# Performance work log

Hardware: AMD Instinct MI355X
Metric: run time of the kernel (lower is better)

## Reference

```python
import jax, jax.numpy as jnp
import numpy as np

TEMP = 0.05
EPS = 1e-6


def _l2norm(x):
    return x / jnp.linalg.norm(x, axis=1, keepdims=True)


def setup_inputs() -> dict:
    key = jax.random.key(0)
    k1, k2, k3, k4 = jax.random.split(key, 4)
    B, D = 4096, 768
    return {
        "feat": jax.random.normal(k1, (B, D), dtype=jnp.float32),
        "feat_gen": jax.random.normal(k2, (B, D), dtype=jnp.float32),
        "feat_aug": jax.random.normal(k3, (B, D), dtype=jnp.float32),
        "targets": jax.random.randint(k4, (B,), 0, 100, dtype=jnp.int64),
    }


def reference(feat, feat_gen, feat_aug, targets):
    B = feat.shape[0]
    on = _l2norm(feat)
    gn = _l2norm(feat_gen)
    an = _l2norm(feat_aug)
    # [B, B] exp-similarity matrices
    exp_ori = jnp.exp(on @ on.T / TEMP)
    exp_gen = jnp.exp(on @ gn.T / TEMP)
    exp_aug = jnp.exp(on @ an.T / TEMP)

    same = (targets[:, None] == targets[None, :])  # [B, B] bool, includes diagonal
    same_f = same.astype(exp_ori.dtype)

    # ---- co loss: anchors vs ori+aug columns ----
    oa = exp_ori + exp_aug
    diff_sum_oa = oa.sum(axis=1) - (oa * same_f).sum(axis=1)        # [B]
    denom_co = diff_sum_oa + exp_gen.sum(axis=1) + EPS              # [B]
    term_o = -jnp.log(exp_ori / (exp_ori + denom_co[:, None]) + EPS)
    term_a = -jnp.log(exp_aug / (exp_aug + denom_co[:, None]) + EPS)
    co_loss = ((term_o + term_a) * same_f).sum() / B

    # ---- ad loss: anchors vs gen columns ----
    diff_sum_g = exp_gen.sum(axis=1) - (exp_gen * same_f).sum(axis=1)
    denom_ad = diff_sum_g + exp_aug.sum(axis=1) + exp_ori.sum(axis=1) + EPS
    term_g = -jnp.log(exp_gen / (exp_gen + denom_ad[:, None]) + EPS)
    ad_loss = (term_g * same_f).sum() / B

    return (ad_loss, co_loss)
```

## Files before the change

### kernel.cpp

```cpp
#include <hip/hip_runtime.h>
#include <hip/hip_bf16.h>
#include <math.h>

#define Bn 4096
#define Dd 768
#define SC2 28.85390081777927f
#define EPSF 1e-6f
#define DG 4.8516519541e8f

#define O_S      0
#define O_SMOA   12288
#define O_SMG    16384
#define ZERO_F   20480
#define O_P      20480
#define O_RM     20608
#define LIST_OFF   262144
#define LCAP       (1u << 19)
#define NB_OFF     33554432

typedef __attribute__((ext_vector_type(8))) short sh8;
typedef __attribute__((ext_vector_type(4))) float f32x4;

#define AS1 __attribute__((address_space(1)))
#define AS3 __attribute__((address_space(3)))

static __device__ __forceinline__ void gl_lds16(const void* g, void* l) {
    __builtin_amdgcn_global_load_lds((const AS1 void*)g, (AS3 void*)l, 16, 0, 0);
}

static __device__ __forceinline__ unsigned short f2b(float f) {
    unsigned int u = __float_as_uint(f);
    unsigned int r = (u + 0x7fffu + ((u >> 16) & 1u)) >> 16;
    return (unsigned short)r;
}

__global__ void norm_kernel(const float* f0, const float* f1, const float* f2, unsigned short* nb) {
    int r = blockIdx.x, m = blockIdx.y, tid = threadIdx.x;
    const float* src = (m == 0 ? f0 : (m == 1 ? f1 : f2)) + (size_t)r * Dd;
    float x0 = src[tid], x1 = src[tid + 256], x2 = src[tid + 512];
    float v = x0 * x0 + x1 * x1 + x2 * x2;
    #pragma unroll
    for (int off = 1; off < 64; off <<= 1) v += __shfl_xor(v, off);
    __shared__ float wr[4];
    if ((tid & 63) == 0) wr[tid >> 6] = v;
    __syncthreads();
    float inv = rsqrtf(wr[0] + wr[1] + wr[2] + wr[3]);
    unsigned short* dst = nb + ((size_t)m * Bn + r) * Dd;
    dst[tid] = f2b(x0 * inv);
    dst[tid + 256] = f2b(x1 * inv);
    dst[tid + 512] = f2b(x2 * inv);
}

__launch_bounds__(1024)
__global__ void sort_kernel(const int* tg, unsigned int* I, float* out) {
    float* F = (float*)I;
    __shared__ unsigned int h[128], pb[128], cur[128];
    int tid = threadIdx.x;
    for (int e = tid; e < ZERO_F; e += 1024) F[e] = 0.f;
    if (tid == 0) { out[0] = 0.f; out[1] = 0.f; }
    if (tid < 128) { h[tid] = 0; cur[tid] = 0; }
    __syncthreads();
    for (int e = tid; e < Bn; e += 1024) atomicAdd(&h[tg[e]], 1u);
    __syncthreads();
    if (tid < 128) pb[tid] = h[tid] * h[tid];
    __syncthreads();
    for (int s = 1; s < 128; s <<= 1) {
        unsigned int b = 0;
        if (tid < 128 && tid >= s) b = pb[tid - s];
        __syncthreads();
        if (tid < 128) pb[tid] += b;
        __syncthreads();
    }
    if (tid == 127) I[O_P] = pb[127];
    uint2* RM = (uint2*)(I + O_RM);
    for (int e = tid; e < Bn; e += 1024) {
        int c = tg[e];
        unsigned int r = atomicAdd(&cur[c], 1u);
        unsigned int n = h[c];
        RM[e] = make_uint2((unsigned)c | (r << 8), (pb[c] - n * n) + r * n);
    }
}

__launch_bounds__(256, 4)
__global__ void gemm_rowsum(const unsigned short* nb, char* ws) {
    float* F = (float*)ws;
    const unsigned int* I = (const unsigned int*)ws;
    const uint2* RM = (const uint2*)(I + O_RM);
    int z = blockIdx.z;
    const unsigned short* Ag = nb;
    const unsigned short* Bg = nb + (size_t)z * Bn * Dd;
    int m0 = blockIdx.y * 128, n0 = blockIdx.x * 128;
    int tid = threadIdx.x, lane = tid & 63, wave = tid >> 6;
    int wm = (wave >> 1) * 64, wn = (wave & 1) * 64;
    int lid = lane & 15, q = lane >> 4;
    __shared__ __align__(16) unsigned short Asm[128 * 32];
    __shared__ __align__(16) unsigned short Bsm[128 * 32];
    int c0 = tid, c1 = tid + 256;
    int row0 = c0 >> 2, sg0 = (c0 & 3) ^ ((row0 >> 1) & 3);
    int row1 = c1 >> 2, sg1 = (c1 & 3) ^ ((row1 >> 1) & 3);
    const unsigned short* gA0 = Ag + (size_t)(m0 + row0) * Dd + sg0 * 8;
    const unsigned short* gA1 = Ag + (size_t)(m0 + row1) * Dd + sg1 * 8;
    const unsigned short* gB0 = Bg + (size_t)(n0 + row0) * Dd + sg0 * 8;
    const unsigned short* gB1 = Bg + (size_t)(n0 + row1) * Dd + sg1 * 8;
    unsigned short* lA0 = &Asm[c0 * 8];
    unsigned short* lA1 = &Asm[c1 * 8];
    unsigned short* lB0 = &Bsm[c0 * 8];
    unsigned short* lB1 = &Bsm[c1 * 8];
    f32x4 acc[4][4] = {};
    for (int kt = 0; kt < Dd / 32; ++kt) {
        __syncthreads();
        gl_lds16(gA0 + kt * 32, lA0);
        gl_lds16(gA1 + kt * 32, lA1);
        gl_lds16(gB0 + kt * 32, lB0);
        gl_lds16(gB1 + kt * 32, lB1);
        __syncthreads();
        sh8 af[4], bf[4];
        #pragma unroll
        for (int i = 0; i < 4; ++i) {
            int r = wm + i * 16 + lid;
            af[i] = *(const sh8*)&Asm[r * 32 + ((q ^ ((r >> 1) & 3)) * 8)];
        }
        #pragma unroll
        for (int j = 0; j < 4; ++j) {
            int r = wn + j * 16 + lid;
            bf[j] = *(const sh8*)&Bsm[r * 32 + ((q ^ ((r >> 1) & 3)) * 8)];
        }
        #pragma unroll
        for (int i = 0; i < 4; ++i)
            #pragma unroll
            for (int j = 0; j < 4; ++j)
                acc[i][j] = __builtin_amdgcn_mfma_f32_16x16x32_bf16(af[i], bf[j], acc[i][j], 0, 0, 0);
    }
    uint2 rmc[4];
    #pragma unroll
    for (int j = 0; j < 4; ++j) rmc[j] = RM[n0 + wn + j * 16 + lid];
    int smoff = (z == 1) ? O_SMG : O_SMOA;
    unsigned int* Lw = (unsigned int*)(ws + LIST_OFF);
    #pragma unroll
    for (int i = 0; i < 4; ++i)
        #pragma unroll
        for (int reg = 0; reg < 4; ++reg) {
            int grow = m0 + wm + i * 16 + q * 4 + reg;
            uint2 rm = RM[grow];
            unsigned int trow = rm.x & 255u, rsb = rm.y;
            float rs = 0.f, ms = 0.f;
            #pragma unroll
            for (int j = 0; j < 4; ++j) {
                int gcol = n0 + wn + j * 16 + lid;
                float x = acc[i][j][reg] * SC2;
                float e = exp2f(x);
                if (z == 0 && gcol == grow) e = 0.f;
                rs += e;
                if ((rmc[j].x & 255u) == trow) {
                    ms += e;
                    unsigned int slot = rsb + (rmc[j].x >> 8);
                    if (slot < LCAP) {
                        if (z == 0) {
                            Lw[slot * 4 + 0] = (unsigned)grow;
                            Lw[slot * 4 + 1] = __float_as_uint(x);
                        } else {
                            Lw[slot * 4 + 1 + z] = __float_as_uint(x);
                        }
                    }
                }
            }
            #pragma unroll
            for (int off = 1; off < 16; off <<= 1) {
                rs += __shfl_xor(rs, off);
                ms += __shfl_xor(ms, off);
            }
            if (lid == 0) {
                atomicAdd(&F[O_S + z * Bn + grow], rs);
                atomicAdd(&F[smoff + grow], ms);
            }
        }
}

__launch_bounds__(256)
__global__ void loss_kernel(char* ws, float* out) {
    float* F = (float*)ws;
    const unsigned int* I = (const unsigned int*)ws;
    const uint4* L = (const uint4*)(ws + LIST_OFF);
    unsigned int n = I[O_P]; if (n > LCAP) n = LCAP;
    float a0 = 0.f, a1 = 0.f;
    unsigned int stride = gridDim.x * 256;
    for (unsigned int idx = blockIdx.x * 256 + threadIdx.x; idx < n; idx += stride) {
        uint4 en = L[idx];
        int i = (int)en.x;
        float son = F[O_S + i], sgen = F[O_S + Bn + i], saug = F[O_S + 2 * Bn + i];
        float dco = (son + saug - F[O_SMOA + i]) + sgen + EPSF;
        float dad = (sgen - F[O_SMG + i]) + saug + son + DG + EPSF;
        float eo = exp2f(__uint_as_float(en.y));
        float eg = exp2f(__uint_as_float(en.z));
        float ea = exp2f(__uint_as_float(en.w));
        a0 += -__logf(eg / (eg + dad) + EPSF);
        a1 += -__logf(eo / (eo + dco) + EPSF) - __logf(ea / (ea + dco) + EPSF);
    }
    #pragma unroll
    for (int off = 1; off < 64; off <<= 1) { a0 += __shfl_xor(a0, off); a1 += __shfl_xor(a1, off); }
    __shared__ float r0[4], r1[4];
    int tid = threadIdx.x;
    if ((tid & 63) == 0) { r0[tid >> 6] = a0; r1[tid >> 6] = a1; }
    __syncthreads();
    if (tid == 0) {
        atomicAdd(&out[0], (r0[0] + r0[1] + r0[2] + r0[3]) * (1.0f / Bn));
        atomicAdd(&out[1], (r1[0] + r1[1] + r1[2] + r1[3]) * (1.0f / Bn));
    }
}

extern "C" void kernel_launch(void* const* d_in, const int* in_sizes, int n_in,
                              void* d_out, int out_size, void* d_ws, size_t ws_size,
                              hipStream_t stream) {
    const float* f0 = (const float*)d_in[0];
    const float* f1 = (const float*)d_in[1];
    const float* f2 = (const float*)d_in[2];
    const int* tg = (const int*)d_in[3];
    char* ws = (char*)d_ws;
    unsigned int* I = (unsigned int*)d_ws;
    unsigned short* nb = (unsigned short*)(ws + NB_OFF);
    float* out = (float*)d_out;

    norm_kernel<<<dim3(Bn, 3), 256, 0, stream>>>(f0, f1, f2, nb);
    sort_kernel<<<1, 1024, 0, stream>>>(tg, I, out);
    gemm_rowsum<<<dim3(32, 32, 3), 256, 0, stream>>>(nb, ws);
    loss_kernel<<<256, 256, 0, stream>>>(ws, out);
}
```

Measured before the change: 221.2 us.

## Enlarge GEMM tile to 256x256 with 4-stage async LDS pipeline

The fused similarity GEMM moves from 128x128 tiles with 256 threads to 256x256 tiles with 512 threads. Each wave now computes 128x64. K-slices are prefetched three steps ahead into four LDS buffers, using explicit vmcnt waits and one barrier per step instead of two. MFMA blocks are wrapped in setprio. This aims to raise operand reuse and hide global-to-LDS latency, at the cost of 128 KB of LDS per block, more accumulator registers, and fewer blocks (768) to spread across CUs.

After: 256.1 us. 1.16x slower.

```diff
diff --git a/kernel.cpp b/kernel.cpp
--- a/kernel.cpp
+++ b/kernel.cpp
@@ -81,7 +81,7 @@
     }
 }
 
-__launch_bounds__(256, 4)
+__launch_bounds__(512, 2)
 __global__ void gemm_rowsum(const unsigned short* nb, char* ws) {
     float* F = (float*)ws;
     const unsigned int* I = (const unsigned int*)ws;
@@ -89,55 +89,74 @@
     int z = blockIdx.z;
     const unsigned short* Ag = nb;
     const unsigned short* Bg = nb + (size_t)z * Bn * Dd;
-    int m0 = blockIdx.y * 128, n0 = blockIdx.x * 128;
+    int m0 = blockIdx.y * 256, n0 = blockIdx.x * 256;
     int tid = threadIdx.x, lane = tid & 63, wave = tid >> 6;
-    int wm = (wave >> 1) * 64, wn = (wave & 1) * 64;
+    int wm = (wave >> 2) * 128, wn = (wave & 3) * 64;
     int lid = lane & 15, q = lane >> 4;
-    __shared__ __align__(16) unsigned short Asm[128 * 32];
-    __shared__ __align__(16) unsigned short Bsm[128 * 32];
-    int c0 = tid, c1 = tid + 256;
-    int row0 = c0 >> 2, sg0 = (c0 & 3) ^ ((row0 >> 1) & 3);
-    int row1 = c1 >> 2, sg1 = (c1 & 3) ^ ((row1 >> 1) & 3);
-    const unsigned short* gA0 = Ag + (size_t)(m0 + row0) * Dd + sg0 * 8;
-    const unsigned short* gA1 = Ag + (size_t)(m0 + row1) * Dd + sg1 * 8;
-    const unsigned short* gB0 = Bg + (size_t)(n0 + row0) * Dd + sg0 * 8;
-    const unsigned short* gB1 = Bg + (size_t)(n0 + row1) * Dd + sg1 * 8;
-    unsigned short* lA0 = &Asm[c0 * 8];
-    unsigned short* lA1 = &Asm[c1 * 8];
-    unsigned short* lB0 = &Bsm[c0 * 8];
-    unsigned short* lB1 = &Bsm[c1 * 8];
-    f32x4 acc[4][4] = {};
-    for (int kt = 0; kt < Dd / 32; ++kt) {
-        __syncthreads();
-        gl_lds16(gA0 + kt * 32, lA0);
-        gl_lds16(gA1 + kt * 32, lA1);
-        gl_lds16(gB0 + kt * 32, lB0);
-        gl_lds16(gB1 + kt * 32, lB1);
-        __syncthreads();
-        sh8 af[4], bf[4];
-        #pragma unroll
-        for (int i = 0; i < 4; ++i) {
+    __shared__ __align__(16) unsigned short Asm[4][256 * 32];
+    __shared__ __align__(16) unsigned short Bsm[4][256 * 32];
+
+    int r0 = tid >> 2, c0 = tid & 3;
+    int sg = (c0 ^ ((r0 >> 1) & 3)) * 8;
+    const unsigned short* pA0 = Ag + (size_t)(m0 + r0) * Dd + sg;
+    const unsigned short* pA1 = pA0 + (size_t)128 * Dd;
+    const unsigned short* pB0 = Bg + (size_t)(n0 + r0) * Dd + sg;
+    const unsigned short* pB1 = pB0 + (size_t)128 * Dd;
+
+    f32x4 acc[8][4] = {};
+
+    #pragma unroll
+    for (int p = 0; p < 3; ++p) {
+        gl_lds16(pA0 + p * 32, &Asm[p][tid * 8]);
+        gl_lds16(pA1 + p * 32, &Asm[p][(512 + tid) * 8]);
+        gl_lds16(pB0 + p * 32, &Bsm[p][tid * 8]);
+        gl_lds16(pB1 + p * 32, &Bsm[p][(512 + tid) * 8]);
+    }
+    pA0 += 96; pA1 += 96; pB0 += 96; pB1 += 96;
+
+    for (int kt = 0; kt < 24; ++kt) {
+        int buf = kt & 3;
+        if (kt < 22)       asm volatile("s_waitcnt vmcnt(8)" ::: "memory");
+        else if (kt == 22) asm volatile("s_waitcnt vmcnt(4)" ::: "memory");
+        else               asm volatile("s_waitcnt vmcnt(0)" ::: "memory");
+        __builtin_amdgcn_sched_barrier(0);
+        __builtin_amdgcn_s_barrier();
+        __builtin_amdgcn_sched_barrier(0);
+        if (kt < 21) {
+            int nbuf = (kt + 3) & 3;
+            gl_lds16(pA0, &Asm[nbuf][tid * 8]);
+            gl_lds16(pA1, &Asm[nbuf][(512 + tid) * 8]);
+            gl_lds16(pB0, &Bsm[nbuf][tid * 8]);
+            gl_lds16(pB1, &Bsm[nbuf][(512 + tid) * 8]);
+            pA0 += 32; pA1 += 32; pB0 += 32; pB1 += 32;
+        }
+        sh8 af[8], bf[4];
+        #pragma unroll
+        for (int i = 0; i < 8; ++i) {
             int r = wm + i * 16 + lid;
-            af[i] = *(const sh8*)&Asm[r * 32 + ((q ^ ((r >> 1) & 3)) * 8)];
+            af[i] = *(const sh8*)&Asm[buf][r * 32 + ((q ^ ((r >> 1) & 3)) * 8)];
         }
         #pragma unroll
         for (int j = 0; j < 4; ++j) {
             int r = wn + j * 16 + lid;
-            bf[j] = *(const sh8*)&Bsm[r * 32 + ((q ^ ((r >> 1) & 3)) * 8)];
-        }
-        #pragma unroll
-        for (int i = 0; i < 4; ++i)
+            bf[j] = *(const sh8*)&Bsm[buf][r * 32 + ((q ^ ((r >> 1) & 3)) * 8)];
+        }
+        __builtin_amdgcn_s_setprio(1);
+        #pragma unroll
+        for (int i = 0; i < 8; ++i)
             #pragma unroll
             for (int j = 0; j < 4; ++j)
                 acc[i][j] = __builtin_amdgcn_mfma_f32_16x16x32_bf16(af[i], bf[j], acc[i][j], 0, 0, 0);
-    }
+        __builtin_amdgcn_s_setprio(0);
+    }
+
     uint2 rmc[4];
     #pragma unroll
     for (int j = 0; j < 4; ++j) rmc[j] = RM[n0 + wn + j * 16 + lid];
     int smoff = (z == 1) ? O_SMG : O_SMOA;
     unsigned int* Lw = (unsigned int*)(ws + LIST_OFF);
     #pragma unroll
-    for (int i = 0; i < 4; ++i)
+    for (int i = 0; i < 8; ++i)
         #pragma unroll
         for (int reg = 0; reg < 4; ++reg) {
             int grow = m0 + wm + i * 16 + q * 4 + reg;
@@ -222,6 +241,6 @@
 
     norm_kernel<<<dim3(Bn, 3), 256, 0, stream>>>(f0, f1, f2, nb);
     sort_kernel<<<1, 1024, 0, stream>>>(tg, I, out);
-    gemm_rowsum<<<dim3(32, 32, 3), 256, 0, stream>>>(nb, ws);
+    gemm_rowsum<<<dim3(16, 16, 3), 512, 0, stream>>>(nb, ws);
     loss_kernel<<<256, 256, 0, stream>>>(ws, out);
 }
```

## Fuse three similarity GEMMs into one block sharing the anchor tile

Applied to the files above, without the earlier changes.

Each block now computes the ori, gen and aug similarity tiles together and loads the anchor A tile once for all three, where before the z dimension launched separate blocks. The epilogue computes all three row sums and same-class sums in one pass and writes each list entry as a single uint4 store instead of scattered partial writes. A swizzled 1D block index is added to improve L2 locality. In exchange the block holds three sets of accumulators (48 f32x4 each), so register pressure rises, launch bounds drop to 2 blocks per SIMD, and there are fewer blocks to spread over the CUs.

New measurement: 205.4 us. 1.08x faster.

```diff
diff --git a/kernel.cpp b/kernel.cpp
--- a/kernel.cpp
+++ b/kernel.cpp
@@ -81,61 +81,91 @@
     }
 }
 
-__launch_bounds__(256, 4)
+__launch_bounds__(256, 2)
 __global__ void gemm_rowsum(const unsigned short* nb, char* ws) {
     float* F = (float*)ws;
     const unsigned int* I = (const unsigned int*)ws;
     const uint2* RM = (const uint2*)(I + O_RM);
-    int z = blockIdx.z;
-    const unsigned short* Ag = nb;
-    const unsigned short* Bg = nb + (size_t)z * Bn * Dd;
-    int m0 = blockIdx.y * 128, n0 = blockIdx.x * 128;
+    int bid = blockIdx.x;
+    int sw = (bid & 7) * 128 + (bid >> 3);
+    int m0 = (sw >> 5) * 128, n0 = (sw & 31) * 128;
     int tid = threadIdx.x, lane = tid & 63, wave = tid >> 6;
     int wm = (wave >> 1) * 64, wn = (wave & 1) * 64;
     int lid = lane & 15, q = lane >> 4;
     __shared__ __align__(16) unsigned short Asm[128 * 32];
-    __shared__ __align__(16) unsigned short Bsm[128 * 32];
-    int c0 = tid, c1 = tid + 256;
-    int row0 = c0 >> 2, sg0 = (c0 & 3) ^ ((row0 >> 1) & 3);
-    int row1 = c1 >> 2, sg1 = (c1 & 3) ^ ((row1 >> 1) & 3);
-    const unsigned short* gA0 = Ag + (size_t)(m0 + row0) * Dd + sg0 * 8;
-    const unsigned short* gA1 = Ag + (size_t)(m0 + row1) * Dd + sg1 * 8;
-    const unsigned short* gB0 = Bg + (size_t)(n0 + row0) * Dd + sg0 * 8;
-    const unsigned short* gB1 = Bg + (size_t)(n0 + row1) * Dd + sg1 * 8;
-    unsigned short* lA0 = &Asm[c0 * 8];
-    unsigned short* lA1 = &Asm[c1 * 8];
-    unsigned short* lB0 = &Bsm[c0 * 8];
-    unsigned short* lB1 = &Bsm[c1 * 8];
-    f32x4 acc[4][4] = {};
-    for (int kt = 0; kt < Dd / 32; ++kt) {
-        __syncthreads();
-        gl_lds16(gA0 + kt * 32, lA0);
-        gl_lds16(gA1 + kt * 32, lA1);
-        gl_lds16(gB0 + kt * 32, lB0);
-        gl_lds16(gB1 + kt * 32, lB1);
-        __syncthreads();
-        sh8 af[4], bf[4];
-        #pragma unroll
-        for (int i = 0; i < 4; ++i) {
-            int r = wm + i * 16 + lid;
-            af[i] = *(const sh8*)&Asm[r * 32 + ((q ^ ((r >> 1) & 3)) * 8)];
-        }
-        #pragma unroll
-        for (int j = 0; j < 4; ++j) {
-            int r = wn + j * 16 + lid;
-            bf[j] = *(const sh8*)&Bsm[r * 32 + ((q ^ ((r >> 1) & 3)) * 8)];
-        }
+    __shared__ __align__(16) unsigned short Bsm[3][128 * 32];
+
+    int row0 = tid >> 2, ch = tid & 3;
+    int cs = (ch ^ ((row0 >> 1) & 3)) * 8;
+    const unsigned short* gA  = nb + (size_t)(m0 + row0) * Dd + cs;
+    const unsigned short* gB0 = nb + (size_t)(n0 + row0) * Dd + cs;
+    const unsigned short* gB1 = gB0 + (size_t)Bn * Dd;
+    const unsigned short* gB2 = gB1 + (size_t)Bn * Dd;
+    unsigned short* lA0 = &Asm[tid * 8];
+    unsigned short* lA1 = &Asm[(tid + 256) * 8];
+
+    int cswz = (q ^ ((lid >> 1) & 3)) * 8;
+
+    f32x4 a0[4][4] = {}, a1[4][4] = {}, a2[4][4] = {};
+
+    for (int kt = 0; kt < 24; ++kt) {
+        const unsigned short* pa  = gA  + kt * 32;
+        const unsigned short* pb0 = gB0 + kt * 32;
+        const unsigned short* pb1 = gB1 + kt * 32;
+        const unsigned short* pb2 = gB2 + kt * 32;
+        __syncthreads();
+        gl_lds16(pa, lA0);
+        gl_lds16(pa + (size_t)64 * Dd, lA1);
+        gl_lds16(pb0, &Bsm[0][tid * 8]);
+        gl_lds16(pb0 + (size_t)64 * Dd, &Bsm[0][(tid + 256) * 8]);
+        gl_lds16(pb1, &Bsm[1][tid * 8]);
+        gl_lds16(pb1 + (size_t)64 * Dd, &Bsm[1][(tid + 256) * 8]);
+        gl_lds16(pb2, &Bsm[2][tid * 8]);
+        gl_lds16(pb2 + (size_t)64 * Dd, &Bsm[2][(tid + 256) * 8]);
+        __syncthreads();
+        sh8 af[4];
         #pragma unroll
         for (int i = 0; i < 4; ++i)
+            af[i] = *(const sh8*)&Asm[(wm + i * 16 + lid) * 32 + cswz];
+        {
+            sh8 bf[4];
             #pragma unroll
             for (int j = 0; j < 4; ++j)
-                acc[i][j] = __builtin_amdgcn_mfma_f32_16x16x32_bf16(af[i], bf[j], acc[i][j], 0, 0, 0);
-    }
+                bf[j] = *(const sh8*)&Bsm[0][(wn + j * 16 + lid) * 32 + cswz];
+            #pragma unroll
+            for (int i = 0; i < 4; ++i)
+                #pragma unroll
+                for (int j = 0; j < 4; ++j)
+                    a0[i][j] = __builtin_amdgcn_mfma_f32_16x16x32_bf16(af[i], bf[j], a0[i][j], 0, 0, 0);
+        }
+        {
+            sh8 bf[4];
+            #pragma unroll
+            for (int j = 0; j < 4; ++j)
+                bf[j] = *(const sh8*)&Bsm[1][(wn + j * 16 + lid) * 32 + cswz];
+            #pragma unroll
+            for (int i = 0; i < 4; ++i)
+                #pragma unroll
+                for (int j = 0; j < 4; ++j)
+                    a1[i][j] = __builtin_amdgcn_mfma_f32_16x16x32_bf16(af[i], bf[j], a1[i][j], 0, 0, 0);
+        }
+        {
+            sh8 bf[4];
+            #pragma unroll
+            for (int j = 0; j < 4; ++j)
+                bf[j] = *(const sh8*)&Bsm[2][(wn + j * 16 + lid) * 32 + cswz];
+            #pragma unroll
+            for (int i = 0; i < 4; ++i)
+                #pragma unroll
+                for (int j = 0; j < 4; ++j)
+                    a2[i][j] = __builtin_amdgcn_mfma_f32_16x16x32_bf16(af[i], bf[j], a2[i][j], 0, 0, 0);
+        }
+    }
+
     uint2 rmc[4];
     #pragma unroll
     for (int j = 0; j < 4; ++j) rmc[j] = RM[n0 + wn + j * 16 + lid];
-    int smoff = (z == 1) ? O_SMG : O_SMOA;
-    unsigned int* Lw = (unsigned int*)(ws + LIST_OFF);
+    uint4* Lq = (uint4*)(ws + LIST_OFF);
     #pragma unroll
     for (int i = 0; i < 4; ++i)
         #pragma unroll
@@ -143,35 +173,41 @@
             int grow = m0 + wm + i * 16 + q * 4 + reg;
             uint2 rm = RM[grow];
             unsigned int trow = rm.x & 255u, rsb = rm.y;
-            float rs = 0.f, ms = 0.f;
+            float rs0 = 0.f, rs1 = 0.f, rs2 = 0.f, msOA = 0.f, msG = 0.f;
             #pragma unroll
             for (int j = 0; j < 4; ++j) {
                 int gcol = n0 + wn + j * 16 + lid;
-                float x = acc[i][j][reg] * SC2;
-                float e = exp2f(x);
-                if (z == 0 && gcol == grow) e = 0.f;
-                rs += e;
+                float x0 = a0[i][j][reg] * SC2;
+                float x1 = a1[i][j][reg] * SC2;
+                float x2 = a2[i][j][reg] * SC2;
+                float e0 = exp2f(x0);
+                float e1 = exp2f(x1);
+                float e2 = exp2f(x2);
+                if (gcol == grow) e0 = 0.f;
+                rs0 += e0; rs1 += e1; rs2 += e2;
                 if ((rmc[j].x & 255u) == trow) {
-                    ms += e;
+                    msOA += e0 + e2;
+                    msG  += e1;
                     unsigned int slot = rsb + (rmc[j].x >> 8);
-                    if (slot < LCAP) {
-                        if (z == 0) {
-                            Lw[slot * 4 + 0] = (unsigned)grow;
-                            Lw[slot * 4 + 1] = __float_as_uint(x);
-                        } else {
-                            Lw[slot * 4 + 1 + z] = __float_as_uint(x);
-                        }
-                    }
+                    if (slot < LCAP)
+                        Lq[slot] = make_uint4((unsigned)grow, __float_as_uint(x0),
+                                              __float_as_uint(x1), __float_as_uint(x2));
                 }
             }
             #pragma unroll
             for (int off = 1; off < 16; off <<= 1) {
-                rs += __shfl_xor(rs, off);
-                ms += __shfl_xor(ms, off);
+                rs0 += __shfl_xor(rs0, off);
+                rs1 += __shfl_xor(rs1, off);
+                rs2 += __shfl_xor(rs2, off);
+                msOA += __shfl_xor(msOA, off);
+                msG  += __shfl_xor(msG, off);
             }
             if (lid == 0) {
-                atomicAdd(&F[O_S + z * Bn + grow], rs);
-                atomicAdd(&F[smoff + grow], ms);
+                atomicAdd(&F[O_S + grow], rs0);
+                atomicAdd(&F[O_S + Bn + grow], rs1);
+                atomicAdd(&F[O_S + 2 * Bn + grow], rs2);
+                atomicAdd(&F[O_SMOA + grow], msOA);
+                atomicAdd(&F[O_SMG + grow], msG);
             }
         }
 }
@@ -222,6 +258,6 @@
 
     norm_kernel<<<dim3(Bn, 3), 256, 0, stream>>>(f0, f1, f2, nb);
     sort_kernel<<<1, 1024, 0, stream>>>(tg, I, out);
-    gemm_rowsum<<<dim3(32, 32, 3), 256, 0, stream>>>(nb, ws);
+    gemm_rowsum<<<dim3(1024), 256, 0, stream>>>(nb, ws);
     loss_kernel<<<256, 256, 0, stream>>>(ws, out);
 }
```

## Share A tile across three similarity GEMMs and fold sort into norm kernel

Applied to the files above, without the earlier changes.

The GEMM now runs one 768-thread block per output tile. Twelve waves split into three groups, one for each of the z matrices (ori, gen, aug). They share a single LDS copy of the A tile instead of reloading it in three separate blocks. Blocks are remapped so that each XCD gets a group of column tiles for L2 locality, and MFMA issue is wrapped in s_setprio. The label-sort kernel is merged into the normalization launch as an extra block, which removes one launch. The cost is lower occupancy (2 blocks of 768 threads) and a larger LDS footprint.

Result: slower. 262.7 us (+18.8%).

```diff
diff --git a/kernel.cpp b/kernel.cpp
--- a/kernel.cpp
+++ b/kernel.cpp
@@ -34,8 +34,39 @@
     return (unsigned short)r;
 }
 
-__global__ void norm_kernel(const float* f0, const float* f1, const float* f2, unsigned short* nb) {
+__global__ void norm_sort_kernel(const float* f0, const float* f1, const float* f2,
+                                 unsigned short* nb, const int* tg, unsigned int* I,
+                                 float* out) {
     int r = blockIdx.x, m = blockIdx.y, tid = threadIdx.x;
+    if (r == Bn) {
+        if (m != 0) return;
+        float* F = (float*)I;
+        __shared__ unsigned int h[128], pb[128], cur[128];
+        for (int e = tid; e < ZERO_F; e += 256) F[e] = 0.f;
+        if (tid == 0) { out[0] = 0.f; out[1] = 0.f; }
+        if (tid < 128) { h[tid] = 0; cur[tid] = 0; }
+        __syncthreads();
+        for (int e = tid; e < Bn; e += 256) atomicAdd(&h[tg[e]], 1u);
+        __syncthreads();
+        if (tid < 128) pb[tid] = h[tid] * h[tid];
+        __syncthreads();
+        for (int s = 1; s < 128; s <<= 1) {
+            unsigned int b = 0;
+            if (tid < 128 && tid >= s) b = pb[tid - s];
+            __syncthreads();
+            if (tid < 128) pb[tid] += b;
+            __syncthreads();
+        }
+        if (tid == 127) I[O_P] = pb[127];
+        uint2* RM = (uint2*)(I + O_RM);
+        for (int e = tid; e < Bn; e += 256) {
+            int c = tg[e];
+            unsigned int rk = atomicAdd(&cur[c], 1u);
+            unsigned int n = h[c];
+            RM[e] = make_uint2((unsigned)c | (rk << 8), (pb[c] - n * n) + rk * n);
+        }
+        return;
+    }
     const float* src = (m == 0 ? f0 : (m == 1 ? f1 : f2)) + (size_t)r * Dd;
     float x0 = src[tid], x1 = src[tid + 256], x2 = src[tid + 512];
     float v = x0 * x0 + x1 * x1 + x2 * x2;
@@ -51,86 +82,59 @@
     dst[tid + 512] = f2b(x2 * inv);
 }
 
-__launch_bounds__(1024)
-__global__ void sort_kernel(const int* tg, unsigned int* I, float* out) {
-    float* F = (float*)I;
-    __shared__ unsigned int h[128], pb[128], cur[128];
-    int tid = threadIdx.x;
-    for (int e = tid; e < ZERO_F; e += 1024) F[e] = 0.f;
-    if (tid == 0) { out[0] = 0.f; out[1] = 0.f; }
-    if (tid < 128) { h[tid] = 0; cur[tid] = 0; }
-    __syncthreads();
-    for (int e = tid; e < Bn; e += 1024) atomicAdd(&h[tg[e]], 1u);
-    __syncthreads();
-    if (tid < 128) pb[tid] = h[tid] * h[tid];
-    __syncthreads();
-    for (int s = 1; s < 128; s <<= 1) {
-        unsigned int b = 0;
-        if (tid < 128 && tid >= s) b = pb[tid - s];
-        __syncthreads();
-        if (tid < 128) pb[tid] += b;
-        __syncthreads();
-    }
-    if (tid == 127) I[O_P] = pb[127];
-    uint2* RM = (uint2*)(I + O_RM);
-    for (int e = tid; e < Bn; e += 1024) {
-        int c = tg[e];
-        unsigned int r = atomicAdd(&cur[c], 1u);
-        unsigned int n = h[c];
-        RM[e] = make_uint2((unsigned)c | (r << 8), (pb[c] - n * n) + r * n);
-    }
-}
-
-__launch_bounds__(256, 4)
+__launch_bounds__(768, 2)
 __global__ void gemm_rowsum(const unsigned short* nb, char* ws) {
     float* F = (float*)ws;
     const unsigned int* I = (const unsigned int*)ws;
     const uint2* RM = (const uint2*)(I + O_RM);
-    int z = blockIdx.z;
-    const unsigned short* Ag = nb;
-    const unsigned short* Bg = nb + (size_t)z * Bn * Dd;
-    int m0 = blockIdx.y * 128, n0 = blockIdx.x * 128;
+    int bid = blockIdx.x;
+    int xcd = bid & 7, local = bid >> 3;
+    int n0 = (xcd * 4 + (local & 3)) * 128;
+    int m0 = (local >> 2) * 128;
     int tid = threadIdx.x, lane = tid & 63, wave = tid >> 6;
-    int wm = (wave >> 1) * 64, wn = (wave & 1) * 64;
+    int z = wave >> 2, sub = wave & 3;
+    int wm = (sub >> 1) * 64, wn = (sub & 1) * 64;
     int lid = lane & 15, q = lane >> 4;
-    __shared__ __align__(16) unsigned short Asm[128 * 32];
-    __shared__ __align__(16) unsigned short Bsm[128 * 32];
-    int c0 = tid, c1 = tid + 256;
-    int row0 = c0 >> 2, sg0 = (c0 & 3) ^ ((row0 >> 1) & 3);
-    int row1 = c1 >> 2, sg1 = (c1 & 3) ^ ((row1 >> 1) & 3);
-    const unsigned short* gA0 = Ag + (size_t)(m0 + row0) * Dd + sg0 * 8;
-    const unsigned short* gA1 = Ag + (size_t)(m0 + row1) * Dd + sg1 * 8;
-    const unsigned short* gB0 = Bg + (size_t)(n0 + row0) * Dd + sg0 * 8;
-    const unsigned short* gB1 = Bg + (size_t)(n0 + row1) * Dd + sg1 * 8;
-    unsigned short* lA0 = &Asm[c0 * 8];
-    unsigned short* lA1 = &Asm[c1 * 8];
-    unsigned short* lB0 = &Bsm[c0 * 8];
-    unsigned short* lB1 = &Bsm[c1 * 8];
+    __shared__ __align__(16) unsigned short L[4][4096];
+
+    int row0 = tid >> 2, ch = tid & 3;
+    int cs = (ch ^ ((row0 >> 1) & 3)) * 8;
+    const unsigned short* gA  = nb + (size_t)(m0 + row0) * Dd + cs;
+    const unsigned short* gB0 = nb + (size_t)(n0 + row0) * Dd + cs;
+    const unsigned short* gB1 = gB0 + (size_t)Bn * Dd;
+    const unsigned short* gB2 = gB1 + (size_t)Bn * Dd;
+
+    int cswz = (q ^ ((lid >> 1) & 3)) * 8;
+    const unsigned short* Bz = &L[1 + z][0];
+
     f32x4 acc[4][4] = {};
-    for (int kt = 0; kt < Dd / 32; ++kt) {
-        __syncthreads();
-        gl_lds16(gA0 + kt * 32, lA0);
-        gl_lds16(gA1 + kt * 32, lA1);
-        gl_lds16(gB0 + kt * 32, lB0);
-        gl_lds16(gB1 + kt * 32, lB1);
+
+    for (int kt = 0; kt < 24; ++kt) {
+        __syncthreads();
+        if (tid < 512) {
+            int ko = kt * 32;
+            gl_lds16(gA  + ko, &L[0][tid * 8]);
+            gl_lds16(gB0 + ko, &L[1][tid * 8]);
+            gl_lds16(gB1 + ko, &L[2][tid * 8]);
+            gl_lds16(gB2 + ko, &L[3][tid * 8]);
+        }
         __syncthreads();
         sh8 af[4], bf[4];
         #pragma unroll
-        for (int i = 0; i < 4; ++i) {
-            int r = wm + i * 16 + lid;
-            af[i] = *(const sh8*)&Asm[r * 32 + ((q ^ ((r >> 1) & 3)) * 8)];
-        }
-        #pragma unroll
-        for (int j = 0; j < 4; ++j) {
-            int r = wn + j * 16 + lid;
-            bf[j] = *(const sh8*)&Bsm[r * 32 + ((q ^ ((r >> 1) & 3)) * 8)];
-        }
+        for (int i = 0; i < 4; ++i)
+            af[i] = *(const sh8*)&L[0][(wm + i * 16 + lid) * 32 + cswz];
+        #pragma unroll
+        for (int j = 0; j < 4; ++j)
+            bf[j] = *(const sh8*)&Bz[(wn + j * 16 + lid) * 32 + cswz];
+        __builtin_amdgcn_s_setprio(1);
         #pragma unroll
         for (int i = 0; i < 4; ++i)
             #pragma unroll
             for (int j = 0; j < 4; ++j)
                 acc[i][j] = __builtin_amdgcn_mfma_f32_16x16x32_bf16(af[i], bf[j], acc[i][j], 0, 0, 0);
-    }
+        __builtin_amdgcn_s_setprio(0);
+    }
+
     uint2 rmc[4];
     #pragma unroll
     for (int j = 0; j < 4; ++j) rmc[j] = RM[n0 + wn + j * 16 + lid];
@@ -220,8 +224,7 @@
     unsigned short* nb = (unsigned short*)(ws + NB_OFF);
     float* out = (float*)d_out;
 
-    norm_kernel<<<dim3(Bn, 3), 256, 0, stream>>>(f0, f1, f2, nb);
-    sort_kernel<<<1, 1024, 0, stream>>>(tg, I, out);
-    gemm_rowsum<<<dim3(32, 32, 3), 256, 0, stream>>>(nb, ws);
+    norm_sort_kernel<<<dim3(Bn + 1, 3), 256, 0, stream>>>(f0, f1, f2, nb, tg, I, out);
+    gemm_rowsum<<<dim3(1024), 768, 0, stream>>>(nb, ws);
     loss_kernel<<<256, 256, 0, stream>>>(ws, out);
 }
```
